# Kernel optimization log

Measured on AMD Instinct MI355X. Metric: run time of the kernel, lower is better.

## Reference

```python
import jax, jax.numpy as jnp
import numpy as np


def _prelu(x, a):
    # torch.nn.PReLU with per-channel parameter a (broadcast over batch)
    return jnp.where(x >= 0, x, a * x)


def setup_inputs() -> dict:
    key = jax.random.key(0)
    ks = jax.random.split(key, 12)
    B = 8192
    dims = [512, 1024, 1024, 512]  # tardim
    E = 8                          # tctrl = modim[-1]
    scale = 0.02                   # keep activations well-scaled across 3 layers
    inp = {
        "x": jax.random.normal(ks[0], (B, dims[0]), dtype=jnp.float32),
        "weights": jax.random.uniform(ks[1], (E,), dtype=jnp.float32),
    }
    for i in range(3):
        din, dout = dims[i], dims[i + 1]
        inp[f"W{i}"] = jax.random.normal(ks[2 + 3 * i], (E, din, dout), dtype=jnp.float32) * scale
        inp[f"b{i}"] = jax.random.normal(ks[3 + 3 * i], (E, dout), dtype=jnp.float32) * scale
        inp[f"a{i}"] = jnp.full((dout,), 0.25, dtype=jnp.float32)  # PReLU init
    return inp


def reference(x, weights, W0, b0, a0, W1, b1, a1, W2, b2, a2):
    # mie.g: per layer, weighted sum over tctrl expert Linears, then PReLU.
    # sum_j (w_j/sum(w)) * (x @ W_j + b_j) == x @ (sum_j wn_j W_j) + sum_j wn_j b_j,
    # so pre-merge expert weights (tiny contraction) and do one GEMM per layer.
    wn = weights / jnp.sum(weights)  # [E]
    for W, b, a in ((W0, b0, a0), (W1, b1, a1), (W2, b2, a2)):
        Wm = jnp.einsum('e,eio->io', wn, W)  # merged weight [in, out]
        bm = jnp.einsum('e,eo->o', wn, b)    # merged bias   [out]
        x = _prelu(x @ Wm + bm, a)           # [B, out]
    return x
```

## Files before the change

### kernel.cpp

```cpp
#include <hip/hip_runtime.h>
#include <stdint.h>

typedef unsigned short u16;
typedef __attribute__((ext_vector_type(8))) short short8;
typedef __attribute__((ext_vector_type(4))) float float4v;

__device__ __forceinline__ u16 f2bf(float f) {
    union { float f; uint32_t u; } v; v.f = f;
    uint32_t r = v.u + 0x7fffu + ((v.u >> 16) & 1u);
    return (u16)(r >> 16);
}

__device__ __forceinline__ void gload16(const u16* g, u16* l) {
    __builtin_amdgcn_global_load_lds(
        (const __attribute__((address_space(1))) void*)g,
        (__attribute__((address_space(3))) void*)l, 16, 0, 0);
}

__global__ __launch_bounds__(256) void prep_fused(
    const float* __restrict__ x, u16* __restrict__ xbf,
    const float* __restrict__ wts,
    const float* __restrict__ W0, const float* __restrict__ W1, const float* __restrict__ W2,
    u16* __restrict__ W0t, u16* __restrict__ W1t, u16* __restrict__ W2t,
    const float* __restrict__ b0, const float* __restrict__ b1, const float* __restrict__ b2,
    float* __restrict__ bm) {
    __shared__ float tile[32][33];
    const int b = blockIdx.x, tid = threadIdx.x;

    if (b < 4096) {
        int i = (b * 256 + tid) * 4;
        float4 v = *(const float4*)(x + i);
        union { u16 s[4]; uint64_t q; } o;
        o.s[0] = f2bf(v.x); o.s[1] = f2bf(v.y); o.s[2] = f2bf(v.z); o.s[3] = f2bf(v.w);
        *(uint64_t*)(xbf + i) = o.q;
        return;
    }

    float wn[8]; float s = 0.f;
    #pragma unroll
    for (int e = 0; e < 8; ++e) { wn[e] = wts[e]; s += wn[e]; }
    const float inv = 1.0f / s;

    if (b < 6144) {
        const float* W; u16* Wt; int K, N, lb;
        if (b < 4608)      { W = W0; Wt = W0t; K = 512;  N = 1024; lb = b - 4096; }
        else if (b < 5632) { W = W1; Wt = W1t; K = 1024; N = 1024; lb = b - 4608; }
        else               { W = W2; Wt = W2t; K = 1024; N = 512;  lb = b - 5632; }
        const int ntiles = N >> 5;
        const int o0 = (lb % ntiles) * 32, i0 = (lb / ntiles) * 32;
        const int tx = tid & 31, ty = tid >> 5;
        #pragma unroll
        for (int s4 = 0; s4 < 4; ++s4) {
            int il = ty + s4 * 8;
            float acc = 0.f;
            #pragma unroll
            for (int e = 0; e < 8; ++e)
                acc += wn[e] * W[(size_t)e * K * N + (size_t)(i0 + il) * N + o0 + tx];
            tile[il][tx] = acc * inv;
        }
        __syncthreads();
        #pragma unroll
        for (int s4 = 0; s4 < 4; ++s4) {
            int ol = ty + s4 * 8;
            Wt[(size_t)(o0 + ol) * K + i0 + tx] = f2bf(tile[tx][ol]);
        }
        return;
    }

    int t = (b - 6144) * 256 + tid;
    if (t >= 2560) return;
    const float* bp; int o, stride;
    if (t < 1024)      { bp = b0; o = t;        stride = 1024; }
    else if (t < 2048) { bp = b1; o = t - 1024; stride = 1024; }
    else               { bp = b2; o = t - 2048; stride = 512;  }
    float acc = 0.f;
    #pragma unroll
    for (int e = 0; e < 8; ++e) acc += wn[e] * bp[e * stride + o];
    bm[t] = acc * inv;
}

template <bool OUT_F32>
__global__ __launch_bounds__(256, 4) void gemm_bias_prelu(
    const u16* __restrict__ A, const u16* __restrict__ Bt,
    const float* __restrict__ bias, const float* __restrict__ alpha,
    void* __restrict__ outp, int M, int N, int K) {
    __shared__ __align__(16) u16 As[128 * 64];
    __shared__ __align__(16) u16 Bs[64 * 64];
    const int tid = threadIdx.x;
    const int bn = blockIdx.x, bm = blockIdx.y;

    const int r0 = tid >> 3;
    const int p  = tid & 7;
    const int c  = p ^ (r0 & 7);
    const u16* Ag = A  + (size_t)(bm * 128 + r0) * K + c * 8;
    const u16* Bg = Bt + (size_t)(bn * 64  + r0) * K + c * 8;
    u16* Al = As + tid * 8;
    u16* Bl = Bs + tid * 8;

    const int lane = tid & 63, w = tid >> 6;
    const int wm = (w >> 1) * 64, wncol = (w & 1) * 32;
    const int l16 = lane & 15, quad = lane >> 4;
    const int xr = l16 & 7;
    const short8* As8 = (const short8*)As;
    const short8* Bs8 = (const short8*)Bs;

    float4v acc[4][2] = {};

    const int nk = K >> 6;
    for (int kt = 0; kt < nk; ++kt) {
        #pragma unroll
        for (int it = 0; it < 4; ++it)
            gload16(Ag + (size_t)(it * 32) * K, Al + it * 2048);
        #pragma unroll
        for (int it = 0; it < 2; ++it)
            gload16(Bg + (size_t)(it * 32) * K, Bl + it * 2048);
        __syncthreads();
        #pragma unroll
        for (int kk = 0; kk < 2; ++kk) {
            const int cb = kk * 4;
            short8 af[4], bf[2];
            #pragma unroll
            for (int mi = 0; mi < 4; ++mi)
                af[mi] = As8[(wm + mi * 16 + l16) * 8 + ((cb + quad) ^ xr)];
            #pragma unroll
            for (int ni = 0; ni < 2; ++ni)
                bf[ni] = Bs8[(wncol + ni * 16 + l16) * 8 + ((cb + quad) ^ xr)];
            #pragma unroll
            for (int mi = 0; mi < 4; ++mi)
                #pragma unroll
                for (int ni = 0; ni < 2; ++ni)
                    acc[mi][ni] = __builtin_amdgcn_mfma_f32_16x16x32_bf16(
                        af[mi], bf[ni], acc[mi][ni], 0, 0, 0);
        }
        if (kt + 1 < nk) __syncthreads();
        Ag += 64; Bg += 64;
    }

    const int cbase = bn * 64 + wncol + l16;
    float bv[2], av[2];
    #pragma unroll
    for (int ni = 0; ni < 2; ++ni) { bv[ni] = bias[cbase + ni * 16]; av[ni] = alpha[cbase + ni * 16]; }
    const int rbase = bm * 128 + wm + quad * 4;
    #pragma unroll
    for (int mi = 0; mi < 4; ++mi) {
        #pragma unroll
        for (int reg = 0; reg < 4; ++reg) {
            int r = rbase + mi * 16 + reg;
            #pragma unroll
            for (int ni = 0; ni < 2; ++ni) {
                float v = acc[mi][ni][reg] + bv[ni];
                v = v >= 0.f ? v : av[ni] * v;
                size_t idx = (size_t)r * N + cbase + ni * 16;
                if (OUT_F32) ((float*)outp)[idx] = v;
                else         ((u16*)outp)[idx] = f2bf(v);
            }
        }
    }
}

extern "C" void kernel_launch(void* const* d_in, const int* in_sizes, int n_in,
                              void* d_out, int out_size, void* d_ws, size_t ws_size,
                              hipStream_t stream) {
    const float* x   = (const float*)d_in[0];
    const float* wts = (const float*)d_in[1];
    const float* W0  = (const float*)d_in[2];
    const float* b0  = (const float*)d_in[3];
    const float* a0  = (const float*)d_in[4];
    const float* W1  = (const float*)d_in[5];
    const float* b1  = (const float*)d_in[6];
    const float* a1  = (const float*)d_in[7];
    const float* W2  = (const float*)d_in[8];
    const float* b2  = (const float*)d_in[9];
    const float* a2  = (const float*)d_in[10];
    float* out = (float*)d_out;

    char* ws = (char*)d_ws;
    u16*   xbf  = (u16*)ws;  ws += (size_t)8192 * 512 * 2;
    u16*   act1 = (u16*)ws;  ws += (size_t)8192 * 1024 * 2;
    u16*   act2 = (u16*)ws;  ws += (size_t)8192 * 1024 * 2;
    u16*   W0t  = (u16*)ws;  ws += (size_t)1024 * 512 * 2;
    u16*   W1t  = (u16*)ws;  ws += (size_t)1024 * 1024 * 2;
    u16*   W2t  = (u16*)ws;  ws += (size_t)512 * 1024 * 2;
    float* bm   = (float*)ws;

    prep_fused<<<6154, 256, 0, stream>>>(x, xbf, wts, W0, W1, W2, W0t, W1t, W2t,
                                         b0, b1, b2, bm);

    gemm_bias_prelu<false><<<dim3(16, 64), 256, 0, stream>>>(xbf,  W0t, bm,        a0, act1, 8192, 1024, 512);
    gemm_bias_prelu<false><<<dim3(16, 64), 256, 0, stream>>>(act1, W1t, bm + 1024, a1, act2, 8192, 1024, 1024);
    gemm_bias_prelu<true ><<<dim3(8, 64),  256, 0, stream>>>(act2, W2t, bm + 2048, a2, out,  8192, 512, 1024);
}
```

Measured before the change: 199.4 us.

## Overlap next-layer weight merge with current GEMM and widen N tile

Moves the expert-weight merge for W1 and W2 out of the prep kernel and into extra blocks appended to the previous layer's GEMM grid, so the merge runs alongside GEMM work instead of before it. The first two GEMMs now use a 128x128 tile (BN=128) with launch bounds lowered to 2 blocks per CU, and the grid is flattened to 1D. The wider tile raises per-block data reuse but increases register pressure and lowers occupancy. The merge blocks share the GEMM kernel's LDS allocation.

```diff
diff --git a/kernel.cpp b/kernel.cpp
--- a/kernel.cpp
+++ b/kernel.cpp
@@ -17,11 +17,40 @@
         (__attribute__((address_space(3))) void*)l, 16, 0, 0);
 }
 
+__device__ __forceinline__ float load_wn(const float* wts, float* wn) {
+    float s = 0.f;
+    #pragma unroll
+    for (int e = 0; e < 8; ++e) { wn[e] = wts[e]; s += wn[e]; }
+    return 1.0f / s;
+}
+
+__device__ __forceinline__ void merge_tile(
+    const float* __restrict__ W, u16* __restrict__ Wt, int K, int N, int lb,
+    const float* wn, float inv, float (*tile)[33], int tid) {
+    const int ntiles = N >> 5;
+    const int o0 = (lb % ntiles) * 32, i0 = (lb / ntiles) * 32;
+    const int tx = tid & 31, ty = tid >> 5;
+    #pragma unroll
+    for (int s4 = 0; s4 < 4; ++s4) {
+        int il = ty + s4 * 8;
+        float acc = 0.f;
+        #pragma unroll
+        for (int e = 0; e < 8; ++e)
+            acc += wn[e] * W[(size_t)e * K * N + (size_t)(i0 + il) * N + o0 + tx];
+        tile[il][tx] = acc * inv;
+    }
+    __syncthreads();
+    #pragma unroll
+    for (int s4 = 0; s4 < 4; ++s4) {
+        int ol = ty + s4 * 8;
+        Wt[(size_t)(o0 + ol) * K + i0 + tx] = f2bf(tile[tx][ol]);
+    }
+}
+
 __global__ __launch_bounds__(256) void prep_fused(
     const float* __restrict__ x, u16* __restrict__ xbf,
     const float* __restrict__ wts,
-    const float* __restrict__ W0, const float* __restrict__ W1, const float* __restrict__ W2,
-    u16* __restrict__ W0t, u16* __restrict__ W1t, u16* __restrict__ W2t,
+    const float* __restrict__ W0, u16* __restrict__ W0t,
     const float* __restrict__ b0, const float* __restrict__ b1, const float* __restrict__ b2,
     float* __restrict__ bm) {
     __shared__ float tile[32][33];
@@ -36,38 +65,14 @@
         return;
     }
 
-    float wn[8]; float s = 0.f;
-    #pragma unroll
-    for (int e = 0; e < 8; ++e) { wn[e] = wts[e]; s += wn[e]; }
-    const float inv = 1.0f / s;
-
-    if (b < 6144) {
-        const float* W; u16* Wt; int K, N, lb;
-        if (b < 4608)      { W = W0; Wt = W0t; K = 512;  N = 1024; lb = b - 4096; }
-        else if (b < 5632) { W = W1; Wt = W1t; K = 1024; N = 1024; lb = b - 4608; }
-        else               { W = W2; Wt = W2t; K = 1024; N = 512;  lb = b - 5632; }
-        const int ntiles = N >> 5;
-        const int o0 = (lb % ntiles) * 32, i0 = (lb / ntiles) * 32;
-        const int tx = tid & 31, ty = tid >> 5;
-        #pragma unroll
-        for (int s4 = 0; s4 < 4; ++s4) {
-            int il = ty + s4 * 8;
-            float acc = 0.f;
-            #pragma unroll
-            for (int e = 0; e < 8; ++e)
-                acc += wn[e] * W[(size_t)e * K * N + (size_t)(i0 + il) * N + o0 + tx];
-            tile[il][tx] = acc * inv;
-        }
-        __syncthreads();
-        #pragma unroll
-        for (int s4 = 0; s4 < 4; ++s4) {
-            int ol = ty + s4 * 8;
-            Wt[(size_t)(o0 + ol) * K + i0 + tx] = f2bf(tile[tx][ol]);
-        }
+    float wn[8]; const float inv = load_wn(wts, wn);
+
+    if (b < 4608) {
+        merge_tile(W0, W0t, 512, 1024, b - 4096, wn, inv, tile, tid);
         return;
     }
 
-    int t = (b - 6144) * 256 + tid;
+    int t = (b - 4608) * 256 + tid;
     if (t >= 2560) return;
     const float* bp; int o, stride;
     if (t < 1024)      { bp = b0; o = t;        stride = 1024; }
@@ -79,32 +84,47 @@
     bm[t] = acc * inv;
 }
 
-template <bool OUT_F32>
-__global__ __launch_bounds__(256, 4) void gemm_bias_prelu(
+template <int BN, bool OUT_F32, bool MERGE>
+__global__ __launch_bounds__(256, 2) void gemm_bias_prelu(
     const u16* __restrict__ A, const u16* __restrict__ Bt,
     const float* __restrict__ bias, const float* __restrict__ alpha,
-    void* __restrict__ outp, int M, int N, int K) {
-    __shared__ __align__(16) u16 As[128 * 64];
-    __shared__ __align__(16) u16 Bs[64 * 64];
+    void* __restrict__ outp, int M, int N, int K,
+    const float* __restrict__ wts, const float* __restrict__ Wm,
+    u16* __restrict__ Wmt, int K2, int N2) {
+    __shared__ __align__(16) u16 sh[(128 + BN) * 64];
     const int tid = threadIdx.x;
-    const int bn = blockIdx.x, bm = blockIdx.y;
+    const int nbn = N / BN;
+    const int nGemm = nbn * (M >> 7);
+    const int bid = blockIdx.x;
+
+    if (MERGE && bid >= nGemm) {
+        float wn[8]; const float inv = load_wn(wts, wn);
+        merge_tile(Wm, Wmt, K2, N2, bid - nGemm, wn, inv, (float(*)[33])(void*)sh, tid);
+        return;
+    }
+
+    const int bn = bid % nbn, bm = bid / nbn;
+    u16* As = sh;
+    u16* Bs = sh + 128 * 64;
 
     const int r0 = tid >> 3;
     const int p  = tid & 7;
     const int c  = p ^ (r0 & 7);
     const u16* Ag = A  + (size_t)(bm * 128 + r0) * K + c * 8;
-    const u16* Bg = Bt + (size_t)(bn * 64  + r0) * K + c * 8;
+    const u16* Bg = Bt + (size_t)(bn * BN  + r0) * K + c * 8;
     u16* Al = As + tid * 8;
     u16* Bl = Bs + tid * 8;
 
     const int lane = tid & 63, w = tid >> 6;
-    const int wm = (w >> 1) * 64, wncol = (w & 1) * 32;
+    constexpr int WN = BN / 2;
+    constexpr int NI = WN / 16;
+    const int wm = (w >> 1) * 64, wncol = (w & 1) * WN;
     const int l16 = lane & 15, quad = lane >> 4;
     const int xr = l16 & 7;
     const short8* As8 = (const short8*)As;
     const short8* Bs8 = (const short8*)Bs;
 
-    float4v acc[4][2] = {};
+    float4v acc[4][NI] = {};
 
     const int nk = K >> 6;
     for (int kt = 0; kt < nk; ++kt) {
@@ -112,23 +132,23 @@
         for (int it = 0; it < 4; ++it)
             gload16(Ag + (size_t)(it * 32) * K, Al + it * 2048);
         #pragma unroll
-        for (int it = 0; it < 2; ++it)
+        for (int it = 0; it < BN / 32; ++it)
             gload16(Bg + (size_t)(it * 32) * K, Bl + it * 2048);
         __syncthreads();
         #pragma unroll
         for (int kk = 0; kk < 2; ++kk) {
             const int cb = kk * 4;
-            short8 af[4], bf[2];
+            short8 af[4], bf[NI];
             #pragma unroll
             for (int mi = 0; mi < 4; ++mi)
                 af[mi] = As8[(wm + mi * 16 + l16) * 8 + ((cb + quad) ^ xr)];
             #pragma unroll
-            for (int ni = 0; ni < 2; ++ni)
+            for (int ni = 0; ni < NI; ++ni)
                 bf[ni] = Bs8[(wncol + ni * 16 + l16) * 8 + ((cb + quad) ^ xr)];
             #pragma unroll
             for (int mi = 0; mi < 4; ++mi)
                 #pragma unroll
-                for (int ni = 0; ni < 2; ++ni)
+                for (int ni = 0; ni < NI; ++ni)
                     acc[mi][ni] = __builtin_amdgcn_mfma_f32_16x16x32_bf16(
                         af[mi], bf[ni], acc[mi][ni], 0, 0, 0);
         }
@@ -136,10 +156,10 @@
         Ag += 64; Bg += 64;
     }
 
-    const int cbase = bn * 64 + wncol + l16;
-    float bv[2], av[2];
-    #pragma unroll
-    for (int ni = 0; ni < 2; ++ni) { bv[ni] = bias[cbase + ni * 16]; av[ni] = alpha[cbase + ni * 16]; }
+    const int cbase = bn * BN + wncol + l16;
+    float bv[NI], av[NI];
+    #pragma unroll
+    for (int ni = 0; ni < NI; ++ni) { bv[ni] = bias[cbase + ni * 16]; av[ni] = alpha[cbase + ni * 16]; }
     const int rbase = bm * 128 + wm + quad * 4;
     #pragma unroll
     for (int mi = 0; mi < 4; ++mi) {
@@ -147,7 +167,7 @@
         for (int reg = 0; reg < 4; ++reg) {
             int r = rbase + mi * 16 + reg;
             #pragma unroll
-            for (int ni = 0; ni < 2; ++ni) {
+            for (int ni = 0; ni < NI; ++ni) {
                 float v = acc[mi][ni][reg] + bv[ni];
                 v = v >= 0.f ? v : av[ni] * v;
                 size_t idx = (size_t)r * N + cbase + ni * 16;
@@ -183,10 +203,17 @@
     u16*   W2t  = (u16*)ws;  ws += (size_t)512 * 1024 * 2;
     float* bm   = (float*)ws;
 
-    prep_fused<<<6154, 256, 0, stream>>>(x, xbf, wts, W0, W1, W2, W0t, W1t, W2t,
-                                         b0, b1, b2, bm);
-
-    gemm_bias_prelu<false><<<dim3(16, 64), 256, 0, stream>>>(xbf,  W0t, bm,        a0, act1, 8192, 1024, 512);
-    gemm_bias_prelu<false><<<dim3(16, 64), 256, 0, stream>>>(act1, W1t, bm + 1024, a1, act2, 8192, 1024, 1024);
-    gemm_bias_prelu<true ><<<dim3(8, 64),  256, 0, stream>>>(act2, W2t, bm + 2048, a2, out,  8192, 512, 1024);
-}
+    prep_fused<<<4618, 256, 0, stream>>>(x, xbf, wts, W0, W0t, b0, b1, b2, bm);
+
+    gemm_bias_prelu<128, false, true><<<512 + 1024, 256, 0, stream>>>(
+        xbf, W0t, bm, a0, act1, 8192, 1024, 512,
+        wts, W1, W1t, 1024, 1024);
+
+    gemm_bias_prelu<128, false, true><<<512 + 512, 256, 0, stream>>>(
+        act1, W1t, bm + 1024, a1, act2, 8192, 1024, 1024,
+        wts, W2, W2t, 1024, 512);
+
+    gemm_bias_prelu<64, true, false><<<512, 256, 0, stream>>>(
+        act2, W2t, bm + 2048, a2, out, 8192, 512, 1024,
+        nullptr, nullptr, nullptr, 0, 0);
+}
```

Result: no change. 197.2 us (-1.1%).
